# Kernel tuning notes

Hardware: AMD Instinct MI355X
Metric: run time of the kernel (lower is better)

## Reference

```python
import jax, jax.numpy as jnp
import numpy as np

NTOKENS = 8192   # max_ntokens
TOPK = 2
H = 1024         # hidden
FFN = 4096       # ffn_hidden = 4*hidden
E = 8            # nexperts
M = NTOKENS * TOPK          # total dispatched rows (flux_m_max)
CAP = M // E                # balanced rows per expert


def setup_inputs() -> dict:
    key = jax.random.key(0)
    k1, k2, k3, k4 = jax.random.split(key, 4)
    x = jax.random.normal(k1, (NTOKENS, H), jnp.float32)
    weight0 = jax.random.normal(k2, (E, H, FFN), jnp.float32) * 0.02
    weight1 = jax.random.normal(k3, (E, FFN, H), jnp.float32) * 0.02
    # Balanced routing: scatter_index[t, k] is the row in the expert-sorted
    # dispatched buffer; a permutation of arange(M) gives exactly CAP rows/expert.
    scatter_index = jax.random.permutation(k4, M).reshape(NTOKENS, TOPK).astype(jnp.int32)
    splits = jnp.full((E,), CAP, dtype=jnp.int32)  # rows per expert, sum == M
    return {"x": x, "weight0": weight0, "weight1": weight1,
            "scatter_index": scatter_index, "splits": splits}


def reference(x, weight0, weight1, scatter_index, splits):
    ntokens, topk = scatter_index.shape
    n_exp, h, ffn = weight0.shape
    m = ntokens * topk
    cap = m // n_exp  # splits are balanced by construction (== splits[e])
    # --- AG-scatter: place each (token, k) replica at its dispatched row ---
    vals = jnp.repeat(x, topk, axis=0)                              # [M, h]
    dispatched = jnp.zeros((m, h), x.dtype).at[scatter_index.reshape(-1)].set(vals)
    xe = dispatched.reshape(n_exp, cap, h)                          # [E, C, h]
    # --- grouped GEMM 0 + exact GELU (torch F.gelu default = erf form) ---
    mid = jax.nn.gelu(jnp.einsum('ech,ehf->ecf', xe, weight0), approximate=False)
    # --- grouped GEMM 1 ---
    ye = jnp.einsum('ecf,efh->ech', mid, weight1).reshape(m, h)     # [M, h]
    # --- gather-RS: combine topk expert outputs per token ---
    return ye[scatter_index].sum(axis=1)                            # [ntokens, h]
```

## Files before the change

kernel.cpp:

```cpp
#include <hip/hip_runtime.h>
#include <hip/hip_bf16.h>
#include <cstdint>

constexpr int NT   = 8192;
constexpr int H    = 1024;
constexpr int FFN  = 4096;
constexpr int E    = 8;
constexpr int M    = NT * 2;
constexpr int CAP  = M / E;

typedef unsigned short u16;
typedef short short8 __attribute__((ext_vector_type(8)));
typedef float f32x4 __attribute__((ext_vector_type(4)));

__device__ __forceinline__ u16 f2bf(float f) {
  union { float f; unsigned u; } c{f};
  unsigned r = (c.u + 0x7FFFu + ((c.u >> 16) & 1u)) >> 16;
  return (u16)r;
}
__device__ __forceinline__ float bf2f(u16 u) {
  union { unsigned u; float f; } c{((unsigned)u) << 16};
  return c.f;
}
__device__ __forceinline__ void async16(const void* g, void* l) {
  auto gp = reinterpret_cast<const __attribute__((address_space(1))) unsigned*>(
      reinterpret_cast<uintptr_t>(g));
  auto lp = reinterpret_cast<__attribute__((address_space(3))) unsigned*>(
      reinterpret_cast<uintptr_t>(l));
  __builtin_amdgcn_global_load_lds(gp, lp, 16, 0, 0);
}

__device__ __forceinline__ float gelu_fast(float x) {
  const float u = x * x;
  const float w = x * (-2.30220795f + -0.102943895f * u);
  return x * __frcp_rn(1.0f + exp2f(w));
}

__device__ __forceinline__ void transpose_body(const float* __restrict__ W,
                                               u16* __restrict__ WT,
                                               int K, int N, int tb,
                                               float (*tile)[65]) {
  const int ntx = N >> 6;
  const int per = ntx * (K >> 6);
  const int e   = tb / per;
  const int rem = tb - e * per;
  const int bx  = rem % ntx;
  const int by  = rem / ntx;
  const float* Wp = W + (size_t)e * K * N;
  u16* Tp = WT + (size_t)e * K * N;
  const int k0 = by * 64, n0 = bx * 64;
  const int tid = threadIdx.x;

  const int u = tid & 15, krb = tid >> 4;
#pragma unroll
  for (int p = 0; p < 4; ++p) {
    const int kr = p * 16 + krb;
    float4 v = *(const float4*)&Wp[(size_t)(k0 + kr) * N + n0 + u * 4];
    tile[kr][u * 4 + 0] = v.x;
    tile[kr][u * 4 + 1] = v.y;
    tile[kr][u * 4 + 2] = v.z;
    tile[kr][u * 4 + 3] = v.w;
  }
  __syncthreads();

  const int n = tid >> 3, cb = tid & 7;
#pragma unroll
  for (int p = 0; p < 2; ++p) {
    const int nn = p * 32 + n;
    u16 pack[8];
#pragma unroll
    for (int j = 0; j < 8; ++j) pack[j] = f2bf(tile[cb * 8 + j][nn]);
    *(short8*)&Tp[(size_t)(n0 + nn) * K + k0 + cb * 8] = *(short8*)pack;
  }
}

__device__ __forceinline__ void scatter_body(const float* __restrict__ x,
                                             const int* __restrict__ sidx,
                                             u16* __restrict__ disp, int b) {
  const int tid = threadIdx.x;
  const int half = tid >> 7;
  const int r = tid & 127;
#pragma unroll
  for (int it = 0; it < 2; ++it) {
    const int t = it * 4096 + b * 2 + half;
    const int r0 = sidx[2 * t + 0];
    const int r1 = sidx[2 * t + 1];
    const float4* xr = (const float4*)(x + (size_t)t * H);
    float4 v0 = xr[r * 2 + 0];
    float4 v1 = xr[r * 2 + 1];
    u16 pk[8] = {f2bf(v0.x), f2bf(v0.y), f2bf(v0.z), f2bf(v0.w),
                 f2bf(v1.x), f2bf(v1.y), f2bf(v1.z), f2bf(v1.w)};
    *(short8*)&disp[(size_t)r0 * H + r * 8] = *(short8*)pk;
    *(short8*)&disp[(size_t)r1 * H + r * 8] = *(short8*)pk;
  }
}

__global__ __launch_bounds__(256)
void pre_kernel(const float* __restrict__ x, const float* __restrict__ w0,
                const float* __restrict__ w1, const int* __restrict__ sidx,
                u16* __restrict__ wt0, u16* __restrict__ wt1,
                u16* __restrict__ disp) {
  __shared__ float tile[64][65];
  const int b = blockIdx.x;
  if (b < 2048) { scatter_body(x, sidx, disp, b); return; }
  if (b < 10240) { transpose_body(w0, wt0, H, FFN, b - 2048, tile); return; }
  transpose_body(w1, wt1, FFN, H, b - 10240, tile);
}

__global__ __launch_bounds__(256)
void transpose_cvt_kernel(const float* __restrict__ W, u16* __restrict__ WT,
                          int K, int N) {
  __shared__ float tile[64][65];
  transpose_body(W, WT, K, N, blockIdx.x, tile);
}

template <bool GELU>
__global__ __launch_bounds__(256)
void gemm_bt_kernel(const u16* __restrict__ A,
                    const u16* __restrict__ Bt,
                    u16* __restrict__ C,
                    int Mn, int Nn, int Kn, int ny) {
  __shared__ __align__(16) u16 lA[128 * 64];
  __shared__ __align__(16) u16 lB[128 * 64];

  const int b = blockIdx.x;
  const int e = b & 7;
  const int t = b >> 3;
  const int q = t & 15, s = t >> 4;
  const int sy = ny >> 2;
  const int sm = s % sy, sn = s / sy;
  const int tm = sm * 4 + (q & 3), tn = sn * 4 + (q >> 2);
  const int m0 = tm * 128, n0 = tn * 128;

  const u16* Ae = A  + (size_t)e * Mn * Kn + (size_t)m0 * Kn;
  const u16* Be = Bt + (size_t)e * Nn * Kn + (size_t)n0 * Kn;
  u16* Ce = C + (size_t)e * Mn * Nn;

  const int tid  = threadIdx.x;
  const int lane = tid & 63;
  const int wave = tid >> 6;
  const int wr = wave >> 1, wc = wave & 1;
  const int lhi = lane >> 4, llo = lane & 15;

  const int sr = lane >> 3;
  const int gc = (lane & 7) ^ sr;

  f32x4 acc[4][4] = {};

  for (int kt = 0; kt < Kn; kt += 64) {
#pragma unroll
    for (int s2 = 0; s2 < 4; ++s2) {
      const int i = wave * 4 + s2;
      const int row = i * 8 + sr;
      async16(Ae + (size_t)row * Kn + kt + gc * 8, &lA[i * 512]);
      async16(Be + (size_t)row * Kn + kt + gc * 8, &lB[i * 512]);
    }
    __syncthreads();

#pragma unroll 1
    for (int ks = 0; ks < 2; ++ks) {
      short8 af[4], bf[4];
#pragma unroll
      for (int i = 0; i < 4; ++i) {
        const int row = wr * 64 + i * 16 + llo;
        const int pc = (ks * 4 + lhi) ^ (llo & 7);
        af[i] = *(const short8*)&lA[row * 64 + pc * 8];
      }
#pragma unroll
      for (int j = 0; j < 4; ++j) {
        const int row = wc * 64 + j * 16 + llo;
        const int pc = (ks * 4 + lhi) ^ (llo & 7);
        bf[j] = *(const short8*)&lB[row * 64 + pc * 8];
      }
#pragma unroll
      for (int i = 0; i < 4; ++i)
#pragma unroll
        for (int j = 0; j < 4; ++j)
          acc[i][j] = __builtin_amdgcn_mfma_f32_16x16x32_bf16(af[i], bf[j], acc[i][j], 0, 0, 0);
    }
    __syncthreads();
  }

#pragma unroll
  for (int i = 0; i < 4; ++i) {
    const int mrow = m0 + wr * 64 + i * 16 + lhi * 4;
#pragma unroll
    for (int j = 0; j < 4; ++j) {
      const int ncol = n0 + wc * 64 + j * 16 + llo;
#pragma unroll
      for (int r = 0; r < 4; ++r) {
        float v = acc[i][j][r];
        if (GELU) v = gelu_fast(v);
        Ce[(size_t)(mrow + r) * Nn + ncol] = f2bf(v);
      }
    }
  }
}

__global__ __launch_bounds__(256)
void gather_sum_kernel(const u16* __restrict__ ye,
                       const int* __restrict__ sidx,
                       float* __restrict__ out) {
  const int tid = threadIdx.x;
  const int half = tid >> 7;
  const int r = tid & 127;
#pragma unroll
  for (int it = 0; it < 2; ++it) {
    const int t = it * 4096 + blockIdx.x * 2 + half;
    const int r0 = sidx[2 * t + 0];
    const int r1 = sidx[2 * t + 1];
    short8 a = *(const short8*)&ye[(size_t)r0 * H + r * 8];
    short8 b = *(const short8*)&ye[(size_t)r1 * H + r * 8];
    float4 s0, s1;
    s0.x = bf2f((u16)a[0]) + bf2f((u16)b[0]);
    s0.y = bf2f((u16)a[1]) + bf2f((u16)b[1]);
    s0.z = bf2f((u16)a[2]) + bf2f((u16)b[2]);
    s0.w = bf2f((u16)a[3]) + bf2f((u16)b[3]);
    s1.x = bf2f((u16)a[4]) + bf2f((u16)b[4]);
    s1.y = bf2f((u16)a[5]) + bf2f((u16)b[5]);
    s1.z = bf2f((u16)a[6]) + bf2f((u16)b[6]);
    s1.w = bf2f((u16)a[7]) + bf2f((u16)b[7]);
    float4* orow = (float4*)(out + (size_t)t * H);
    orow[r * 2 + 0] = s0;
    orow[r * 2 + 1] = s1;
  }
}

extern "C" void kernel_launch(void* const* d_in, const int* in_sizes, int n_in,
                              void* d_out, int out_size, void* d_ws, size_t ws_size,
                              hipStream_t stream) {
  (void)in_sizes; (void)n_in; (void)out_size;
  const float* x    = (const float*)d_in[0];
  const float* w0   = (const float*)d_in[1];
  const float* w1   = (const float*)d_in[2];
  const int*   sidx = (const int*)d_in[3];
  float* out = (float*)d_out;

  char* ws = (char*)d_ws;
  const size_t MB = 1024ull * 1024;
  u16* wt0  = (u16*)ws;
  u16* wt1  = (u16*)(ws + 64 * MB);
  u16* disp = (u16*)(ws + 128 * MB);
  u16* mid  = (u16*)(ws + 160 * MB);
  u16* ye   = disp;
  const bool roomy = ws_size >= 288 * MB;

  if (roomy) {
    pre_kernel<<<18432, 256, 0, stream>>>(x, w0, w1, sidx, wt0, wt1, disp);
    gemm_bt_kernel<true><<<4096, 256, 0, stream>>>(disp, wt0, mid, CAP, FFN, H, CAP / 128);
    gemm_bt_kernel<false><<<1024, 256, 0, stream>>>(mid, wt1, ye, CAP, H, FFN, CAP / 128);
  } else {
    wt1 = wt0;
    pre_kernel<<<10240, 256, 0, stream>>>(x, w0, w1, sidx, wt0, wt1, disp);
    gemm_bt_kernel<true><<<4096, 256, 0, stream>>>(disp, wt0, mid, CAP, FFN, H, CAP / 128);
    transpose_cvt_kernel<<<8192, 256, 0, stream>>>(w1, wt1, FFN, H);
    gemm_bt_kernel<false><<<1024, 256, 0, stream>>>(mid, wt1, ye, CAP, H, FFN, CAP / 128);
  }
  gather_sum_kernel<<<2048, 256, 0, stream>>>(ye, sidx, out);
}
```

Measured before the change: 681.1 us.

## Rewrite grouped GEMM with 256x256 tiles, 512 threads and double-buffered LDS pipeline

Replaces the 128x128 single-buffered GEMM with a 256x256 tile per 512-thread block. The K loop is double-buffered and staged into quarter-steps, so global async loads overlap MFMA work. It interleaves LDS fragment loads with barriers and priority hints. This cuts global memory traffic per FLOP and hides load latency, but grid sizes shrink sharply and LDS use rises to 128KB, which limits occupancy.

```diff
diff --git a/kernel.cpp b/kernel.cpp
--- a/kernel.cpp
+++ b/kernel.cpp
@@ -115,13 +115,13 @@
 }
 
 template <bool GELU>
-__global__ __launch_bounds__(256)
+__global__ __launch_bounds__(512, 2)
 void gemm_bt_kernel(const u16* __restrict__ A,
                     const u16* __restrict__ Bt,
                     u16* __restrict__ C,
                     int Mn, int Nn, int Kn, int ny) {
-  __shared__ __align__(16) u16 lA[128 * 64];
-  __shared__ __align__(16) u16 lB[128 * 64];
+  __shared__ __align__(16) u16 lA[2 * 16384];
+  __shared__ __align__(16) u16 lB[2 * 16384];
 
   const int b = blockIdx.x;
   const int e = b & 7;
@@ -130,66 +130,164 @@
   const int sy = ny >> 2;
   const int sm = s % sy, sn = s / sy;
   const int tm = sm * 4 + (q & 3), tn = sn * 4 + (q >> 2);
-  const int m0 = tm * 128, n0 = tn * 128;
-
-  const u16* Ae = A  + (size_t)e * Mn * Kn + (size_t)m0 * Kn;
-  const u16* Be = Bt + (size_t)e * Nn * Kn + (size_t)n0 * Kn;
-  u16* Ce = C + (size_t)e * Mn * Nn;
+  const int m0 = tm * 256, n0 = tn * 256;
+
+  const u16* __restrict__ Ae = A  + (size_t)e * Mn * Kn + (size_t)m0 * Kn;
+  const u16* __restrict__ Be = Bt + (size_t)e * Nn * Kn + (size_t)n0 * Kn;
+  u16* __restrict__ Ce = C + (size_t)e * Mn * Nn;
 
   const int tid  = threadIdx.x;
   const int lane = tid & 63;
   const int wave = tid >> 6;
-  const int wr = wave >> 1, wc = wave & 1;
-  const int lhi = lane >> 4, llo = lane & 15;
-
-  const int sr = lane >> 3;
-  const int gc = (lane & 7) ^ sr;
-
-  f32x4 acc[4][4] = {};
-
-  for (int kt = 0; kt < Kn; kt += 64) {
-#pragma unroll
-    for (int s2 = 0; s2 < 4; ++s2) {
-      const int i = wave * 4 + s2;
-      const int row = i * 8 + sr;
-      async16(Ae + (size_t)row * Kn + kt + gc * 8, &lA[i * 512]);
-      async16(Be + (size_t)row * Kn + kt + gc * 8, &lB[i * 512]);
-    }
-    __syncthreads();
+  const int wr = wave >> 2, wc = wave & 3;
+  const int llo = lane & 15, lhi = lane >> 4, lsw = llo & 7;
+
+  const int gcol = ((tid & 7) ^ ((tid >> 3) & 7)) * 8;
+  const int rowA = tid >> 3;
+  const int rowB = (wave >> 2) * 64 + (wave & 3) * 8 + ((tid >> 3) & 7);
+  const u16* pA = Ae + (size_t)rowA * Kn + gcol;
+  const u16* pB = Be + (size_t)rowB * Kn + gcol;
+  const int ldA = wave * 8 * 64;
+  const int ldB = ((wave >> 2) * 64 + (wave & 3) * 8) * 64;
+
+  const int arow0 = (wr * 128 + llo) * 64;
+  const int brow0 = (wc * 64 + llo) * 64;
+  const int ck0 = (lhi ^ lsw) * 8;
+  const int ck1 = ((lhi + 4) ^ lsw) * 8;
+
+  const int KT  = Kn >> 6;
+  const int KT4 = Kn >> 4;
+
+  auto stage = [&](int n) {
+    if (n >= KT4) return;
+    const int mt = n >> 2, idx = n & 3;
+    const int h = idx >> 1;
+    const int koff = mt << 6;
+    const int bsel = (mt & 1) << 14;
+    if ((idx & 1) == 0) {
+      const u16* sp = pA + (size_t)(h * 64) * Kn + koff;
+      u16* dp = lA + bsel + h * (64 * 64) + ldA;
+      async16(sp, dp);
+      async16(sp + (size_t)128 * Kn, dp + 128 * 64);
+    } else {
+      const u16* sp = pB + (size_t)(h * 32) * Kn + koff;
+      u16* dp = lB + bsel + h * (32 * 64) + ldB;
+      async16(sp, dp);
+      async16(sp + (size_t)128 * Kn, dp + 128 * 64);
+    }
+  };
+
+  f32x4 acc[8][4] = {};
+  short8 aA[4][2], b0f[2][2], b1f[2][2];
+
+#pragma unroll
+  for (int n = 0; n < 7; ++n) stage(n);
+  asm volatile("s_waitcnt vmcnt(6)" ::: "memory");
+  __builtin_amdgcn_s_barrier();
 
 #pragma unroll 1
-    for (int ks = 0; ks < 2; ++ks) {
-      short8 af[4], bf[4];
-#pragma unroll
-      for (int i = 0; i < 4; ++i) {
-        const int row = wr * 64 + i * 16 + llo;
-        const int pc = (ks * 4 + lhi) ^ (llo & 7);
-        af[i] = *(const short8*)&lA[row * 64 + pc * 8];
-      }
-#pragma unroll
-      for (int j = 0; j < 4; ++j) {
-        const int row = wc * 64 + j * 16 + llo;
-        const int pc = (ks * 4 + lhi) ^ (llo & 7);
-        bf[j] = *(const short8*)&lB[row * 64 + pc * 8];
-      }
-#pragma unroll
-      for (int i = 0; i < 4; ++i)
-#pragma unroll
-        for (int j = 0; j < 4; ++j)
-          acc[i][j] = __builtin_amdgcn_mfma_f32_16x16x32_bf16(af[i], bf[j], acc[i][j], 0, 0, 0);
-    }
-    __syncthreads();
-  }
-
-#pragma unroll
-  for (int i = 0; i < 4; ++i) {
-    const int mrow = m0 + wr * 64 + i * 16 + lhi * 4;
-#pragma unroll
-    for (int j = 0; j < 4; ++j) {
-      const int ncol = n0 + wc * 64 + j * 16 + llo;
+  for (int k = 0; k < KT; ++k) {
+    const u16* bA = &lA[(k & 1) << 14];
+    const u16* bB = &lB[(k & 1) << 14];
+    const int g = 4 * k;
+
+#pragma unroll
+    for (int mi = 0; mi < 4; ++mi) {
+      aA[mi][0] = *(const short8*)&bA[arow0 + mi * 1024 + ck0];
+      aA[mi][1] = *(const short8*)&bA[arow0 + mi * 1024 + ck1];
+    }
+#pragma unroll
+    for (int nj = 0; nj < 2; ++nj) {
+      b0f[nj][0] = *(const short8*)&bB[brow0 + nj * 1024 + ck0];
+      b0f[nj][1] = *(const short8*)&bB[brow0 + nj * 1024 + ck1];
+    }
+    stage(g + 7);
+    asm volatile("s_waitcnt lgkmcnt(8)" ::: "memory");
+    __builtin_amdgcn_s_barrier();
+    asm volatile("s_waitcnt lgkmcnt(0)" ::: "memory");
+    __builtin_amdgcn_s_setprio(1);
+#pragma unroll
+    for (int mi = 0; mi < 4; ++mi)
+#pragma unroll
+      for (int nj = 0; nj < 2; ++nj)
+#pragma unroll
+        for (int ks = 0; ks < 2; ++ks)
+          acc[mi][nj] = __builtin_amdgcn_mfma_f32_16x16x32_bf16(
+              aA[mi][ks], b0f[nj][ks], acc[mi][nj], 0, 0, 0);
+    __builtin_amdgcn_s_setprio(0);
+    __builtin_amdgcn_s_barrier();
+
+#pragma unroll
+    for (int nj = 0; nj < 2; ++nj) {
+      b1f[nj][0] = *(const short8*)&bB[brow0 + (nj + 2) * 1024 + ck0];
+      b1f[nj][1] = *(const short8*)&bB[brow0 + (nj + 2) * 1024 + ck1];
+    }
+    stage(g + 8);
+    __builtin_amdgcn_s_barrier();
+    asm volatile("s_waitcnt lgkmcnt(0)" ::: "memory");
+    __builtin_amdgcn_s_setprio(1);
+#pragma unroll
+    for (int mi = 0; mi < 4; ++mi)
+#pragma unroll
+      for (int nj = 0; nj < 2; ++nj)
+#pragma unroll
+        for (int ks = 0; ks < 2; ++ks)
+          acc[mi][nj + 2] = __builtin_amdgcn_mfma_f32_16x16x32_bf16(
+              aA[mi][ks], b1f[nj][ks], acc[mi][nj + 2], 0, 0, 0);
+    __builtin_amdgcn_s_setprio(0);
+    __builtin_amdgcn_s_barrier();
+
+#pragma unroll
+    for (int mi = 0; mi < 4; ++mi) {
+      aA[mi][0] = *(const short8*)&bA[arow0 + (mi + 4) * 1024 + ck0];
+      aA[mi][1] = *(const short8*)&bA[arow0 + (mi + 4) * 1024 + ck1];
+    }
+    stage(g + 9);
+    __builtin_amdgcn_s_barrier();
+    asm volatile("s_waitcnt lgkmcnt(0)" ::: "memory");
+    __builtin_amdgcn_s_setprio(1);
+#pragma unroll
+    for (int mi = 0; mi < 4; ++mi)
+#pragma unroll
+      for (int nj = 0; nj < 2; ++nj)
+#pragma unroll
+        for (int ks = 0; ks < 2; ++ks)
+          acc[mi + 4][nj + 2] = __builtin_amdgcn_mfma_f32_16x16x32_bf16(
+              aA[mi][ks], b1f[nj][ks], acc[mi + 4][nj + 2], 0, 0, 0);
+    __builtin_amdgcn_s_setprio(0);
+    __builtin_amdgcn_s_barrier();
+
+    stage(g + 10);
+    __builtin_amdgcn_s_barrier();
+    __builtin_amdgcn_s_setprio(1);
+#pragma unroll
+    for (int mi = 0; mi < 4; ++mi)
+#pragma unroll
+      for (int nj = 0; nj < 2; ++nj)
+#pragma unroll
+        for (int ks = 0; ks < 2; ++ks)
+          acc[mi + 4][nj] = __builtin_amdgcn_mfma_f32_16x16x32_bf16(
+              aA[mi][ks], b0f[nj][ks], acc[mi + 4][nj], 0, 0, 0);
+    __builtin_amdgcn_s_setprio(0);
+
+    if (k + 2 < KT) {
+      asm volatile("s_waitcnt vmcnt(6)" ::: "memory");
+      __builtin_amdgcn_s_barrier();
+    } else if (k + 2 == KT) {
+      asm volatile("s_waitcnt vmcnt(0)" ::: "memory");
+      __builtin_amdgcn_s_barrier();
+    }
+  }
+
+#pragma unroll
+  for (int mi = 0; mi < 8; ++mi) {
+    const int mrow = m0 + wr * 128 + mi * 16 + lhi * 4;
+#pragma unroll
+    for (int nj = 0; nj < 4; ++nj) {
+      const int ncol = n0 + wc * 64 + nj * 16 + llo;
 #pragma unroll
       for (int r = 0; r < 4; ++r) {
-        float v = acc[i][j][r];
+        float v = acc[mi][nj][r];
         if (GELU) v = gelu_fast(v);
         Ce[(size_t)(mrow + r) * Nn + ncol] = f2bf(v);
       }
@@ -247,14 +345,14 @@
 
   if (roomy) {
     pre_kernel<<<18432, 256, 0, stream>>>(x, w0, w1, sidx, wt0, wt1, disp);
-    gemm_bt_kernel<true><<<4096, 256, 0, stream>>>(disp, wt0, mid, CAP, FFN, H, CAP / 128);
-    gemm_bt_kernel<false><<<1024, 256, 0, stream>>>(mid, wt1, ye, CAP, H, FFN, CAP / 128);
+    gemm_bt_kernel<true><<<1024, 512, 0, stream>>>(disp, wt0, mid, CAP, FFN, H, CAP / 256);
+    gemm_bt_kernel<false><<<256, 512, 0, stream>>>(mid, wt1, ye, CAP, H, FFN, CAP / 256);
   } else {
     wt1 = wt0;
     pre_kernel<<<10240, 256, 0, stream>>>(x, w0, w1, sidx, wt0, wt1, disp);
-    gemm_bt_kernel<true><<<4096, 256, 0, stream>>>(disp, wt0, mid, CAP, FFN, H, CAP / 128);
+    gemm_bt_kernel<true><<<1024, 512, 0, stream>>>(disp, wt0, mid, CAP, FFN, H, CAP / 256);
     transpose_cvt_kernel<<<8192, 256, 0, stream>>>(w1, wt1, FFN, H);
-    gemm_bt_kernel<false><<<1024, 256, 0, stream>>>(mid, wt1, ye, CAP, H, FFN, CAP / 128);
+    gemm_bt_kernel<false><<<256, 512, 0, stream>>>(mid, wt1, ye, CAP, H, FFN, CAP / 256);
   }
   gather_sum_kernel<<<2048, 256, 0, stream>>>(ye, sidx, out);
 }
```

After: 614.0 us. 9.9% less time.
